# Performance work log

Hardware: AMD Instinct MI355X
Metric: run time of the kernel (lower is better)

## Reference

```python
import jax, jax.numpy as jnp
import numpy as np

N, F_IN, HID, C = 50000, 256, 64, 40
E = 1_600_000
EPS = 1e-8  # torch cosine_similarity eps


def setup_inputs() -> dict:
    key = jax.random.key(0)
    ks = jax.random.split(key, 6)
    x = jax.random.normal(ks[0], (N, F_IN), jnp.float32)
    edge_index = jax.random.randint(ks[1], (2, E), 0, N, dtype=jnp.int64)
    edge_weights = jax.random.uniform(ks[2], (E,), jnp.float32)
    W1 = jax.random.normal(ks[3], (F_IN, HID), jnp.float32) / np.float32(np.sqrt(F_IN))
    b1 = jnp.zeros((HID,), jnp.float32)
    W2 = jax.random.normal(ks[4], (HID, C), jnp.float32) / np.float32(np.sqrt(HID))
    b2 = jnp.zeros((C,), jnp.float32)
    return {"x": x, "edge_index": edge_index, "edge_weights": edge_weights,
            "W1": W1, "b1": b1, "W2": W2, "b2": b2}


def _gcn_conv(x, W, b, src, dst, n):
    # PyG GCNConv: out = D^{-1/2} (A + I) D^{-1/2} (X W) + b
    xw = x @ W  # [n, out]
    loops = jnp.arange(n, dtype=src.dtype)
    s = jnp.concatenate([src, loops])  # self-loops appended
    d = jnp.concatenate([dst, loops])
    deg = jax.ops.segment_sum(jnp.ones_like(s, dtype=xw.dtype), d, num_segments=n)
    dinv = jnp.where(deg > 0, jax.lax.rsqrt(jnp.maximum(deg, 1.0)), 0.0)
    norm = dinv[s] * dinv[d]  # [E+n]
    msg = xw[s] * norm[:, None]  # gather + scale (irregular access)
    out = jax.ops.segment_sum(msg, d, num_segments=n)  # scatter-add
    return out + b


def reference(x, edge_index, edge_weights, W1, b1, W2, b2):
    src, dst = edge_index[0], edge_index[1]
    n = x.shape[0]
    # layer 1 + relu (dropout = identity in eval)
    h = jax.nn.relu(_gcn_conv(x, W1, b1, src, dst, n))
    x_out = _gcn_conv(h, W2, b2, src, dst, n)  # [n, C]
    # edge-wise cosine dissimilarity: 1 - cos(x_out[src], x_out[dst])
    a = x_out[src]
    b = x_out[dst]
    na = jnp.maximum(jnp.sqrt(jnp.sum(a * a, axis=-1)), EPS)
    nb = jnp.maximum(jnp.sqrt(jnp.sum(b * b, axis=-1)), EPS)
    cosine_sim = 1.0 - jnp.sum(a * b, axis=-1) / (na * nb)
    gnn_edge = jnp.where(edge_weights > 0.5, 1.0, -1.0)
    return (jax.nn.log_softmax(x_out, axis=1), x_out, cosine_sim, gnn_edge,
            jax.nn.softmax(x_out, axis=1))
```

## Files before the change

kernel.cpp:

```cpp
#include <hip/hip_runtime.h>
#include <hip/hip_bf16.h>

#define F_IN 256
#define HID  64
#define CLS  40
#define EPS  1e-8f
#define XS_STRIDE 264
#define EPB  8192

typedef unsigned short ushort_t;
typedef unsigned int   uint_t;
typedef __attribute__((ext_vector_type(8))) short bf16x8;
typedef __attribute__((ext_vector_type(4))) float f32x4;

__device__ __forceinline__ float bf2f(ushort_t u) {
    union { uint_t i; float f; } v; v.i = ((uint_t)u) << 16; return v.f;
}
__device__ __forceinline__ ushort_t f2bf(float f) {
    union { float f; uint_t i; } v; v.f = f;
    uint_t r = v.i + 0x7fff + ((v.i >> 16) & 1);
    return (ushort_t)(r >> 16);
}
__device__ __forceinline__ float blo(uint_t p) {
    union { uint_t i; float f; } v; v.i = p << 16; return v.f;
}
__device__ __forceinline__ float bhi(uint_t p) {
    union { uint_t i; float f; } v; v.i = p & 0xffff0000u; return v.f;
}
__device__ __forceinline__ float dot_u4(uint4 a, uint4 b) {
    return blo(a.x) * blo(b.x) + bhi(a.x) * bhi(b.x)
         + blo(a.y) * blo(b.y) + bhi(a.y) * bhi(b.y)
         + blo(a.z) * blo(b.z) + bhi(a.z) * bhi(b.z)
         + blo(a.w) * blo(b.w) + bhi(a.w) * bhi(b.w);
}

__global__ void detect_kernel(const int* __restrict__ raw, int* __restrict__ flag) {
    int c = threadIdx.x;
    int w = raw[2 * c + 1];
    unsigned long long b = __ballot(w != 0);
    if (c == 0) *flag = (b == 0ULL) ? 1 : 0;
}

__global__ void build_hist_kernel(const void* __restrict__ raw, const int* __restrict__ flag,
                                  uint_t* __restrict__ pair, int* __restrict__ ghist, int E) {
    __shared__ int lhist[256];
    int tid = threadIdx.x;
    lhist[tid] = 0;
    __syncthreads();
    int base = blockIdx.x * EPB;
    if (*flag) {
        const long long* r = (const long long*)raw;
        for (int it = 0; it < EPB / 1024; ++it) {
            int e = base + (it * 256 + tid) * 4;
            if (e + 4 <= E) {
                ulonglong2 a0 = *(const ulonglong2*)(r + e);
                ulonglong2 a1 = *(const ulonglong2*)(r + e + 2);
                ulonglong2 b0 = *(const ulonglong2*)(r + E + e);
                ulonglong2 b1 = *(const ulonglong2*)(r + E + e + 2);
                uint_t d0 = (uint_t)b0.x, d1 = (uint_t)b0.y;
                uint_t d2 = (uint_t)b1.x, d3 = (uint_t)b1.y;
                uint4 p;
                p.x = (d0 << 16) | (uint_t)a0.x;
                p.y = (d1 << 16) | (uint_t)a0.y;
                p.z = (d2 << 16) | (uint_t)a1.x;
                p.w = (d3 << 16) | (uint_t)a1.y;
                *(uint4*)(pair + e) = p;
                atomicAdd(&lhist[d0 >> 8], 1);
                atomicAdd(&lhist[d1 >> 8], 1);
                atomicAdd(&lhist[d2 >> 8], 1);
                atomicAdd(&lhist[d3 >> 8], 1);
            } else {
                for (int k = 0; k < 4; ++k) {
                    int ee = e + k;
                    if (ee < E) {
                        uint_t s = (uint_t)r[ee];
                        uint_t d = (uint_t)r[E + ee];
                        pair[ee] = (d << 16) | s;
                        atomicAdd(&lhist[d >> 8], 1);
                    }
                }
            }
        }
    } else {
        const int* r = (const int*)raw;
        for (int it = 0; it < EPB / 1024; ++it) {
            int e = base + (it * 256 + tid) * 4;
            if (e + 4 <= E) {
                int4 a = *(const int4*)(r + e);
                int4 b = *(const int4*)(r + E + e);
                uint_t d0 = (uint_t)b.x, d1 = (uint_t)b.y;
                uint_t d2 = (uint_t)b.z, d3 = (uint_t)b.w;
                uint4 p;
                p.x = (d0 << 16) | (uint_t)a.x;
                p.y = (d1 << 16) | (uint_t)a.y;
                p.z = (d2 << 16) | (uint_t)a.z;
                p.w = (d3 << 16) | (uint_t)a.w;
                *(uint4*)(pair + e) = p;
                atomicAdd(&lhist[d0 >> 8], 1);
                atomicAdd(&lhist[d1 >> 8], 1);
                atomicAdd(&lhist[d2 >> 8], 1);
                atomicAdd(&lhist[d3 >> 8], 1);
            } else {
                for (int k = 0; k < 4; ++k) {
                    int ee = e + k;
                    if (ee < E) {
                        uint_t s = (uint_t)r[ee];
                        uint_t d = (uint_t)r[E + ee];
                        pair[ee] = (d << 16) | s;
                        atomicAdd(&lhist[d >> 8], 1);
                    }
                }
            }
        }
    }
    __syncthreads();
    ghist[blockIdx.x * 256 + tid] = lhist[tid];
}

__global__ void scan_cols_kernel(int* __restrict__ ghist, int* __restrict__ btot,
                                 int NBLK) {
    int k    = blockIdx.x;
    int lane = threadIdx.x;
    int carry = 0;
    for (int b0 = 0; b0 < NBLK; b0 += 64) {
        int b = b0 + lane;
        int v = (b < NBLK) ? ghist[b * 256 + k] : 0;
        int x = v;
        #pragma unroll
        for (int o = 1; o < 64; o <<= 1) {
            int t = __shfl_up(x, o);
            if (lane >= o) x += t;
        }
        if (b < NBLK) ghist[b * 256 + k] = carry + x - v;
        carry += __shfl(x, 63);
    }
    if (lane == 0) btot[k] = carry;
}

__global__ void scan_base_kernel(const int* __restrict__ btot, int* __restrict__ bbase) {
    __shared__ int s[256];
    int k = threadIdx.x;
    int v = btot[k];
    int x = v;
    s[k] = x;
    __syncthreads();
    #pragma unroll
    for (int o = 1; o < 256; o <<= 1) {
        int t = (k >= o) ? s[k - o] : 0;
        __syncthreads();
        x += t;
        s[k] = x;
        __syncthreads();
    }
    bbase[k] = x - v;
    if (k == 255) bbase[256] = x;
}

__global__ void scatter_buckets_kernel(const uint_t* __restrict__ pair,
                                       const int* __restrict__ ghist,
                                       const int* __restrict__ bbase,
                                       uint_t* __restrict__ bkt, int E) {
    __shared__ int cursor[256];
    int tid = threadIdx.x;
    cursor[tid] = ghist[blockIdx.x * 256 + tid] + bbase[tid];
    __syncthreads();
    int base = blockIdx.x * EPB;
    for (int it = 0; it < EPB / 256; ++it) {
        int e = base + it * 256 + tid;
        if (e < E) {
            uint_t u = pair[e];
            int pos = atomicAdd(&cursor[u >> 24], 1);
            bkt[pos] = u;
        }
    }
}

__global__ void bucket_csr_kernel(const uint_t* __restrict__ bkt,
                                  const int* __restrict__ bbase,
                                  ushort_t* __restrict__ csr, int* __restrict__ rowptr,
                                  float* __restrict__ dinv, int n, int E, int NBUCK) {
    __shared__ int lhist[256];
    __shared__ int lscan[256];
    __shared__ int cursor[256];
    int tid = threadIdx.x;
    int kb  = blockIdx.x;
    int base = bbase[kb];
    int cnt  = bbase[kb + 1] - base;
    lhist[tid] = 0;
    __syncthreads();
    for (int i = tid; i < cnt; i += 256) {
        uint_t u = bkt[base + i];
        atomicAdd(&lhist[(u >> 16) & 255], 1);
    }
    __syncthreads();
    int v = lhist[tid];
    int x = v;
    lscan[tid] = x;
    __syncthreads();
    #pragma unroll
    for (int o = 1; o < 256; o <<= 1) {
        int t = (tid >= o) ? lscan[tid - o] : 0;
        __syncthreads();
        x += t;
        lscan[tid] = x;
        __syncthreads();
    }
    int excl = x - v;
    int node = kb * 256 + tid;
    if (node < n) {
        rowptr[node] = base + excl;
        dinv[node]   = rsqrtf((float)(v + 1));
    }
    cursor[tid] = base + excl;
    if (kb == NBUCK - 1 && tid == 0) rowptr[n] = E;
    __syncthreads();
    for (int i = tid; i < cnt; i += 256) {
        uint_t u = bkt[base + i];
        int pos = atomicAdd(&cursor[(u >> 16) & 255], 1);
        csr[pos] = (ushort_t)(u & 0xffffu);
    }
}

__global__ void convert_w1_kernel(const float* __restrict__ W1, ushort_t* __restrict__ W1s) {
    int t = blockIdx.x * blockDim.x + threadIdx.x;
    if (t >= 4 * 8 * 64) return;
    int lane = t & 63;
    int kk   = (t >> 6) & 7;
    int nt   = t >> 9;
    int col  = nt * 16 + (lane & 15);
    int k0   = kk * 32 + (lane >> 4) * 8;
    ushort_t v[8];
    #pragma unroll
    for (int j = 0; j < 8; ++j) v[j] = f2bf(W1[(size_t)(k0 + j) * HID + col]);
    uint4 p;
    p.x = (uint_t)v[0] | ((uint_t)v[1] << 16);
    p.y = (uint_t)v[2] | ((uint_t)v[3] << 16);
    p.z = (uint_t)v[4] | ((uint_t)v[5] << 16);
    p.w = (uint_t)v[6] | ((uint_t)v[7] << 16);
    *(uint4*)(W1s + (size_t)t * 8) = p;
}

__global__ void gemm1_mfma_kernel(const float* __restrict__ x,
                                  const ushort_t* __restrict__ W1s,
                                  const float* __restrict__ dinv,
                                  ushort_t* __restrict__ xws, int n) {
    __shared__ ushort_t xs[16 * XS_STRIDE];
    int node0 = blockIdx.x * 16;
    int tid = threadIdx.x;
    for (int i = tid; i < 16 * 64; i += 256) {
        int r  = i >> 6;
        int c4 = (i & 63) << 2;
        int node = node0 + r;
        float4 v = (node < n) ? *(const float4*)(x + (size_t)node * F_IN + c4)
                              : make_float4(0.f, 0.f, 0.f, 0.f);
        ushort4 b;
        b.x = f2bf(v.x); b.y = f2bf(v.y); b.z = f2bf(v.z); b.w = f2bf(v.w);
        *(ushort4*)(&xs[r * XS_STRIDE + c4]) = b;
    }
    __syncthreads();
    int wave = tid >> 6;
    int lane = tid & 63;
    int m    = lane & 15;
    int q    = lane >> 4;
    f32x4 acc = {0.f, 0.f, 0.f, 0.f};
    #pragma unroll
    for (int kk = 0; kk < 8; ++kk) {
        bf16x8 a = *(const bf16x8*)(&xs[m * XS_STRIDE + kk * 32 + q * 8]);
        bf16x8 b = *(const bf16x8*)(W1s + (((size_t)wave * 8 + kk) * 64 + lane) * 8);
        acc = __builtin_amdgcn_mfma_f32_16x16x32_bf16(a, b, acc, 0, 0, 0);
    }
    int ch = wave * 16 + m;
    #pragma unroll
    for (int r = 0; r < 4; ++r) {
        int node = node0 + q * 4 + r;
        if (node < n)
            xws[(size_t)node * HID + ch] = f2bf(acc[r] * dinv[node]);
    }
}

__global__ void gather1_gemm2_kernel(const int* __restrict__ rowptr,
                                     const ushort_t* __restrict__ csr,
                                     const ushort_t* __restrict__ xws,
                                     const float* __restrict__ dinv,
                                     const float* __restrict__ b1,
                                     const float* __restrict__ W2,
                                     ushort_t* __restrict__ hws, int n) {
    __shared__ float hbuf[4][72];
    __shared__ float w2s[HID * CLS];
    int tid  = threadIdx.x;
    int wave = tid >> 6;
    int l    = tid & 63;
    int g    = l >> 3;
    int lc   = l & 7;
    for (int i = tid; i < HID * CLS / 4; i += 256)
        *(float4*)(&w2s[i * 4]) = *(const float4*)(W2 + i * 4);
    int wv = (blockIdx.x * blockDim.x + tid) >> 6;
    bool active = wv < n;
    int beg = 0, endp = 0;
    float di = 0.f;
    float acc8[8];
    #pragma unroll
    for (int j = 0; j < 8; ++j) acc8[j] = 0.f;
    if (active) {
        beg = rowptr[wv]; endp = rowptr[wv + 1];
        di  = dinv[wv];
        if (l < 8) {
            uint4 sv = *(const uint4*)(xws + (size_t)wv * HID + lc * 8);
            acc8[0] = blo(sv.x); acc8[1] = bhi(sv.x);
            acc8[2] = blo(sv.y); acc8[3] = bhi(sv.y);
            acc8[4] = blo(sv.z); acc8[5] = bhi(sv.z);
            acc8[6] = blo(sv.w); acc8[7] = bhi(sv.w);
        }
    }
    for (int ch = beg; ch < endp; ch += 32) {
        #pragma unroll
        for (int k = 0; k < 4; ++k) {
            int e = ch + k * 8 + g;
            bool val = e < endp;
            int ec = val ? e : (endp - 1);
            int s = (int)csr[ec];
            uint4 p = *(const uint4*)(xws + (size_t)s * HID + lc * 8);
            if (!val) { p.x = 0u; p.y = 0u; p.z = 0u; p.w = 0u; }
            acc8[0] += blo(p.x); acc8[1] += bhi(p.x);
            acc8[2] += blo(p.y); acc8[3] += bhi(p.y);
            acc8[4] += blo(p.z); acc8[5] += bhi(p.z);
            acc8[6] += blo(p.w); acc8[7] += bhi(p.w);
        }
    }
    #pragma unroll
    for (int j = 0; j < 8; ++j) {
        float v = acc8[j];
        v += __shfl_xor(v, 8);
        v += __shfl_xor(v, 16);
        v += __shfl_xor(v, 32);
        acc8[j] = v;
    }
    if (active && l < 8) {
        #pragma unroll
        for (int j = 0; j < 8; ++j)
            hbuf[wave][lc * 8 + j] = fmaxf(acc8[j] * di + b1[lc * 8 + j], 0.f);
    }
    __syncthreads();
    if (active) {
        if (l < CLS) {
            float o = 0.f;
            const float* hr = hbuf[wave];
            #pragma unroll 16
            for (int k = 0; k < HID; ++k) o += hr[k] * w2s[k * CLS + l];
            hws[(size_t)wv * HID + l] = f2bf(o * di);
        } else {
            hws[(size_t)wv * HID + l] = 0;
        }
    }
}

__global__ void gather2_fin_kernel(const int* __restrict__ rowptr,
                                   const ushort_t* __restrict__ csr,
                                   const ushort_t* __restrict__ hws,
                                   const float* __restrict__ dinv,
                                   const float* __restrict__ b2,
                                   float* __restrict__ xout, float* __restrict__ lsm,
                                   float* __restrict__ sm, ushort_t* __restrict__ xnb,
                                   int n) {
    int tid = threadIdx.x;
    int wv  = (blockIdx.x * blockDim.x + tid) >> 6;
    if (wv >= n) return;
    int l  = tid & 63;
    int g  = l >> 3;
    int lc = l & 7;
    int beg = rowptr[wv], endp = rowptr[wv + 1];
    float di = dinv[wv];
    float acc8[8];
    #pragma unroll
    for (int j = 0; j < 8; ++j) acc8[j] = 0.f;
    if (l < 8) {
        uint4 sv = *(const uint4*)(hws + (size_t)wv * HID + lc * 8);
        acc8[0] = blo(sv.x); acc8[1] = bhi(sv.x);
        acc8[2] = blo(sv.y); acc8[3] = bhi(sv.y);
        acc8[4] = blo(sv.z); acc8[5] = bhi(sv.z);
        acc8[6] = blo(sv.w); acc8[7] = bhi(sv.w);
    }
    for (int ch = beg; ch < endp; ch += 32) {
        #pragma unroll
        for (int k = 0; k < 4; ++k) {
            int e = ch + k * 8 + g;
            bool val = e < endp;
            int ec = val ? e : (endp - 1);
            int s = (int)csr[ec];
            uint4 p = *(const uint4*)(hws + (size_t)s * HID + lc * 8);
            if (!val) { p.x = 0u; p.y = 0u; p.z = 0u; p.w = 0u; }
            acc8[0] += blo(p.x); acc8[1] += bhi(p.x);
            acc8[2] += blo(p.y); acc8[3] += bhi(p.y);
            acc8[4] += blo(p.z); acc8[5] += bhi(p.z);
            acc8[6] += blo(p.w); acc8[7] += bhi(p.w);
        }
    }
    #pragma unroll
    for (int j = 0; j < 8; ++j) {
        float v = acc8[j];
        v += __shfl_xor(v, 8);
        v += __shfl_xor(v, 16);
        v += __shfl_xor(v, 32);
        acc8[j] = v;
    }
    bool cgv = lc < 5;
    float raw[8];
    if (cgv) {
        #pragma unroll
        for (int j = 0; j < 8; ++j) raw[j] = acc8[j] * di + b2[lc * 8 + j];
    } else {
        #pragma unroll
        for (int j = 0; j < 8; ++j) raw[j] = 0.f;
    }
    float mx = -3.0e38f;
    if (cgv) {
        #pragma unroll
        for (int j = 0; j < 8; ++j) mx = fmaxf(mx, raw[j]);
    }
    mx = fmaxf(mx, __shfl_xor(mx, 1));
    mx = fmaxf(mx, __shfl_xor(mx, 2));
    mx = fmaxf(mx, __shfl_xor(mx, 4));
    float ex[8];
    float ls = 0.f;
    if (cgv) {
        #pragma unroll
        for (int j = 0; j < 8; ++j) { ex[j] = __expf(raw[j] - mx); ls += ex[j]; }
    } else {
        #pragma unroll
        for (int j = 0; j < 8; ++j) ex[j] = 0.f;
    }
    ls += __shfl_xor(ls, 1);
    ls += __shfl_xor(ls, 2);
    ls += __shfl_xor(ls, 4);
    float sq = 0.f;
    if (cgv) {
        #pragma unroll
        for (int j = 0; j < 8; ++j) sq += raw[j] * raw[j];
    }
    sq += __shfl_xor(sq, 1);
    sq += __shfl_xor(sq, 2);
    sq += __shfl_xor(sq, 4);
    float rn = 1.0f / fmaxf(sqrtf(sq), EPS);
    if (l < 5) {
        size_t fb = (size_t)wv * CLS + l * 8;
        *(float4*)(xout + fb)     = make_float4(raw[0], raw[1], raw[2], raw[3]);
        *(float4*)(xout + fb + 4) = make_float4(raw[4], raw[5], raw[6], raw[7]);
        float lse = mx + __logf(ls);
        *(float4*)(lsm + fb)     = make_float4(raw[0] - lse, raw[1] - lse, raw[2] - lse, raw[3] - lse);
        *(float4*)(lsm + fb + 4) = make_float4(raw[4] - lse, raw[5] - lse, raw[6] - lse, raw[7] - lse);
        float inv = 1.0f / ls;
        *(float4*)(sm + fb)     = make_float4(ex[0] * inv, ex[1] * inv, ex[2] * inv, ex[3] * inv);
        *(float4*)(sm + fb + 4) = make_float4(ex[4] * inv, ex[5] * inv, ex[6] * inv, ex[7] * inv);
        uint4 pb;
        pb.x = (uint_t)f2bf(raw[0] * rn) | ((uint_t)f2bf(raw[1] * rn) << 16);
        pb.y = (uint_t)f2bf(raw[2] * rn) | ((uint_t)f2bf(raw[3] * rn) << 16);
        pb.z = (uint_t)f2bf(raw[4] * rn) | ((uint_t)f2bf(raw[5] * rn) << 16);
        pb.w = (uint_t)f2bf(raw[6] * rn) | ((uint_t)f2bf(raw[7] * rn) << 16);
        *(uint4*)(xnb + fb) = pb;
    }
}

__global__ void edge_kernel(const uint_t* __restrict__ pair,
                            const float* __restrict__ ew, const ushort_t* __restrict__ xnb,
                            float* __restrict__ cos_out, float* __restrict__ gnn_out, int E) {
    int tid = threadIdx.x;
    int wid = (blockIdx.x * blockDim.x + tid) >> 6;
    int l = tid & 63;
    int g = l >> 3;
    int j = l & 7;
    int e0 = wid * 32;
    if (e0 >= E) return;
    uint_t u[4];
    #pragma unroll
    for (int k = 0; k < 4; ++k) {
        int e = e0 + k * 8 + g;
        u[k] = (e < E) ? pair[e] : pair[E - 1];
    }
    uint4 av[4], bv[4];
    #pragma unroll
    for (int k = 0; k < 4; ++k) {
        int s = (int)(u[k] & 0xffffu);
        int d = (int)(u[k] >> 16);
        if (j < 5) {
            av[k] = *(const uint4*)(xnb + (size_t)s * CLS + j * 8);
            bv[k] = *(const uint4*)(xnb + (size_t)d * CLS + j * 8);
        }
    }
    #pragma unroll
    for (int k = 0; k < 4; ++k) {
        float part = 0.f;
        if (j < 5) part = dot_u4(av[k], bv[k]);
        part += __shfl_xor(part, 1);
        part += __shfl_xor(part, 2);
        part += __shfl_xor(part, 4);
        int e = e0 + k * 8 + g;
        if (j == 0 && e < E) {
            cos_out[e] = 1.0f - part;
            gnn_out[e] = (ew[e] > 0.5f) ? 1.0f : -1.0f;
        }
    }
}

extern "C" void kernel_launch(void* const* d_in, const int* in_sizes, int n_in,
                              void* d_out, int out_size, void* d_ws, size_t ws_size,
                              hipStream_t stream) {
    const float* x   = (const float*)d_in[0];
    const void*  ei  = d_in[1];
    const float* ew  = (const float*)d_in[2];
    const float* W1  = (const float*)d_in[3];
    const float* b1  = (const float*)d_in[4];
    const float* W2  = (const float*)d_in[5];
    const float* b2  = (const float*)d_in[6];

    const int n = in_sizes[0] / F_IN;
    const int E = in_sizes[2];

    float* lsm  = (float*)d_out;
    float* xout = lsm + (size_t)n * CLS;
    float* cosO = xout + (size_t)n * CLS;
    float* gnnO = cosO + E;
    float* smO  = gnnO + E;

    char* w = (char*)d_ws;
    auto alloc = [&](size_t bytes) {
        char* p = w;
        w += (bytes + 255) & ~(size_t)255;
        return p;
    };
    const int NBLK  = (E + EPB - 1) / EPB;
    const int NBUCK = (n + 255) / 256;

    uint_t*   pair   = (uint_t*)  alloc((size_t)E * 4);
    uint_t*   bkt    = (uint_t*)  alloc((size_t)E * 4);
    ushort_t* csr16  = (ushort_t*)alloc((size_t)E * 2);
    int*      ghist  = (int*)     alloc((size_t)NBLK * 256 * 4);
    int*      btot   = (int*)     alloc(256 * 4);
    int*      bbase  = (int*)     alloc(257 * 4);
    int*      rowptr = (int*)     alloc(((size_t)n + 1) * 4);
    float*    dinv   = (float*)   alloc((size_t)n * 4);
    ushort_t* xws    = (ushort_t*)alloc((size_t)n * HID * 2);
    ushort_t* hws    = (ushort_t*)alloc((size_t)n * HID * 2);
    ushort_t* xnb    = (ushort_t*)alloc((size_t)n * CLS * 2);
    ushort_t* W1s    = (ushort_t*)alloc((size_t)4 * 8 * 64 * 8 * 2);
    int*      flag   = (int*)     alloc(64);

    detect_kernel<<<1, 64, 0, stream>>>((const int*)ei, flag);
    convert_w1_kernel<<<8, 256, 0, stream>>>(W1, W1s);
    build_hist_kernel<<<NBLK, 256, 0, stream>>>(ei, flag, pair, ghist, E);
    scan_cols_kernel<<<256, 64, 0, stream>>>(ghist, btot, NBLK);
    scan_base_kernel<<<1, 256, 0, stream>>>(btot, bbase);
    scatter_buckets_kernel<<<NBLK, 256, 0, stream>>>(pair, ghist, bbase, bkt, E);
    bucket_csr_kernel<<<NBUCK, 256, 0, stream>>>(bkt, bbase, csr16, rowptr, dinv, n, E, NBUCK);
    gemm1_mfma_kernel<<<(n + 15) / 16, 256, 0, stream>>>(x, W1s, dinv, xws, n);
    gather1_gemm2_kernel<<<((size_t)n * 64 + 255) / 256, 256, 0, stream>>>(rowptr, csr16, xws, dinv,
                                                                           b1, W2, hws, n);
    gather2_fin_kernel<<<((size_t)n * 64 + 255) / 256, 256, 0, stream>>>(rowptr, csr16, hws, dinv, b2,
                                                                         xout, lsm, smO, xnb, n);
    edge_kernel<<<((size_t)((E + 31) / 32) * 64 + 255) / 256, 256, 0, stream>>>(pair, ew, xnb, cosO, gnnO, E);
}
```

Measured before the change: 286.1 us.

## Split gather1 from GEMM2 and run GEMM2 on MFMA bf16

The fused gather1+GEMM2 kernel, which staged W2 (10 KB) into shared memory in every 256-thread block and did a scalar 64x40 dot per node with a block-wide sync, is split in two. A gather-only kernel now writes relu(h) as bf16, and a new MFMA kernel computes h·W2 with W2 pre-packed into bf16 fragments (columns padded to 64). This removes the per-block W2 load and the scalar FMA loop. In exchange it adds one launch plus an extra write and read of an n×64 bf16 intermediate, and h is rounded to bf16 before the second GEMM.

```diff
diff --git a/kernel.cpp b/kernel.cpp
--- a/kernel.cpp
+++ b/kernel.cpp
@@ -6,6 +6,7 @@
 #define CLS  40
 #define EPS  1e-8f
 #define XS_STRIDE 264
+#define H2_STRIDE 72
 #define EPB  8192
 
 typedef unsigned short ushort_t;
@@ -240,6 +241,26 @@
     *(uint4*)(W1s + (size_t)t * 8) = p;
 }
 
+__global__ void convert_w2_kernel(const float* __restrict__ W2, ushort_t* __restrict__ W2s) {
+    int t = blockIdx.x * blockDim.x + threadIdx.x;
+    if (t >= 4 * 2 * 64) return;
+    int lane = t & 63;
+    int kk   = (t >> 6) & 1;
+    int nt   = t >> 7;
+    int col  = nt * 16 + (lane & 15);
+    int k0   = kk * 32 + (lane >> 4) * 8;
+    ushort_t v[8];
+    #pragma unroll
+    for (int j = 0; j < 8; ++j)
+        v[j] = (col < CLS) ? f2bf(W2[(size_t)(k0 + j) * CLS + col]) : (ushort_t)0;
+    uint4 p;
+    p.x = (uint_t)v[0] | ((uint_t)v[1] << 16);
+    p.y = (uint_t)v[2] | ((uint_t)v[3] << 16);
+    p.z = (uint_t)v[4] | ((uint_t)v[5] << 16);
+    p.w = (uint_t)v[6] | ((uint_t)v[7] << 16);
+    *(uint4*)(W2s + (size_t)t * 8) = p;
+}
+
 __global__ void gemm1_mfma_kernel(const float* __restrict__ x,
                                   const ushort_t* __restrict__ W1s,
                                   const float* __restrict__ dinv,
@@ -278,39 +299,29 @@
     }
 }
 
-__global__ void gather1_gemm2_kernel(const int* __restrict__ rowptr,
-                                     const ushort_t* __restrict__ csr,
-                                     const ushort_t* __restrict__ xws,
-                                     const float* __restrict__ dinv,
-                                     const float* __restrict__ b1,
-                                     const float* __restrict__ W2,
-                                     ushort_t* __restrict__ hws, int n) {
-    __shared__ float hbuf[4][72];
-    __shared__ float w2s[HID * CLS];
-    int tid  = threadIdx.x;
-    int wave = tid >> 6;
-    int l    = tid & 63;
-    int g    = l >> 3;
-    int lc   = l & 7;
-    for (int i = tid; i < HID * CLS / 4; i += 256)
-        *(float4*)(&w2s[i * 4]) = *(const float4*)(W2 + i * 4);
-    int wv = (blockIdx.x * blockDim.x + tid) >> 6;
-    bool active = wv < n;
-    int beg = 0, endp = 0;
-    float di = 0.f;
+__global__ void gather1_kernel(const int* __restrict__ rowptr,
+                               const ushort_t* __restrict__ csr,
+                               const ushort_t* __restrict__ xws,
+                               const float* __restrict__ dinv,
+                               const float* __restrict__ b1,
+                               ushort_t* __restrict__ h, int n) {
+    int tid = threadIdx.x;
+    int wv  = (blockIdx.x * blockDim.x + tid) >> 6;
+    if (wv >= n) return;
+    int l  = tid & 63;
+    int g  = l >> 3;
+    int lc = l & 7;
+    int beg = rowptr[wv], endp = rowptr[wv + 1];
+    float di = dinv[wv];
     float acc8[8];
     #pragma unroll
     for (int j = 0; j < 8; ++j) acc8[j] = 0.f;
-    if (active) {
-        beg = rowptr[wv]; endp = rowptr[wv + 1];
-        di  = dinv[wv];
-        if (l < 8) {
-            uint4 sv = *(const uint4*)(xws + (size_t)wv * HID + lc * 8);
-            acc8[0] = blo(sv.x); acc8[1] = bhi(sv.x);
-            acc8[2] = blo(sv.y); acc8[3] = bhi(sv.y);
-            acc8[4] = blo(sv.z); acc8[5] = bhi(sv.z);
-            acc8[6] = blo(sv.w); acc8[7] = bhi(sv.w);
-        }
+    if (l < 8) {
+        uint4 sv = *(const uint4*)(xws + (size_t)wv * HID + lc * 8);
+        acc8[0] = blo(sv.x); acc8[1] = bhi(sv.x);
+        acc8[2] = blo(sv.y); acc8[3] = bhi(sv.y);
+        acc8[4] = blo(sv.z); acc8[5] = bhi(sv.z);
+        acc8[6] = blo(sv.w); acc8[7] = bhi(sv.w);
     }
     for (int ch = beg; ch < endp; ch += 32) {
         #pragma unroll
@@ -335,22 +346,59 @@
         v += __shfl_xor(v, 32);
         acc8[j] = v;
     }
-    if (active && l < 8) {
-        #pragma unroll
-        for (int j = 0; j < 8; ++j)
-            hbuf[wave][lc * 8 + j] = fmaxf(acc8[j] * di + b1[lc * 8 + j], 0.f);
-    }
-    __syncthreads();
-    if (active) {
-        if (l < CLS) {
-            float o = 0.f;
-            const float* hr = hbuf[wave];
-            #pragma unroll 16
-            for (int k = 0; k < HID; ++k) o += hr[k] * w2s[k * CLS + l];
-            hws[(size_t)wv * HID + l] = f2bf(o * di);
-        } else {
-            hws[(size_t)wv * HID + l] = 0;
-        }
+    if (l < 8) {
+        float4 bb0 = *(const float4*)(b1 + lc * 8);
+        float4 bb1 = *(const float4*)(b1 + lc * 8 + 4);
+        float h0 = fmaxf(acc8[0] * di + bb0.x, 0.f);
+        float h1 = fmaxf(acc8[1] * di + bb0.y, 0.f);
+        float h2 = fmaxf(acc8[2] * di + bb0.z, 0.f);
+        float h3 = fmaxf(acc8[3] * di + bb0.w, 0.f);
+        float h4 = fmaxf(acc8[4] * di + bb1.x, 0.f);
+        float h5 = fmaxf(acc8[5] * di + bb1.y, 0.f);
+        float h6 = fmaxf(acc8[6] * di + bb1.z, 0.f);
+        float h7 = fmaxf(acc8[7] * di + bb1.w, 0.f);
+        uint4 pb;
+        pb.x = (uint_t)f2bf(h0) | ((uint_t)f2bf(h1) << 16);
+        pb.y = (uint_t)f2bf(h2) | ((uint_t)f2bf(h3) << 16);
+        pb.z = (uint_t)f2bf(h4) | ((uint_t)f2bf(h5) << 16);
+        pb.w = (uint_t)f2bf(h6) | ((uint_t)f2bf(h7) << 16);
+        *(uint4*)(h + (size_t)wv * HID + lc * 8) = pb;
+    }
+}
+
+__global__ void gemm2_mfma_kernel(const ushort_t* __restrict__ h,
+                                  const ushort_t* __restrict__ W2s,
+                                  const float* __restrict__ dinv,
+                                  ushort_t* __restrict__ hws, int n) {
+    __shared__ ushort_t hs[16 * H2_STRIDE];
+    int node0 = blockIdx.x * 16;
+    int tid = threadIdx.x;
+    {
+        int r  = tid >> 4;
+        int c4 = (tid & 15) << 2;
+        int node = node0 + r;
+        ushort4 v = make_ushort4(0, 0, 0, 0);
+        if (node < n) v = *(const ushort4*)(h + (size_t)node * HID + c4);
+        *(ushort4*)(&hs[r * H2_STRIDE + c4]) = v;
+    }
+    __syncthreads();
+    int wave = tid >> 6;
+    int lane = tid & 63;
+    int m    = lane & 15;
+    int q    = lane >> 4;
+    f32x4 acc = {0.f, 0.f, 0.f, 0.f};
+    #pragma unroll
+    for (int kk = 0; kk < 2; ++kk) {
+        bf16x8 a = *(const bf16x8*)(&hs[m * H2_STRIDE + kk * 32 + q * 8]);
+        bf16x8 b = *(const bf16x8*)(W2s + (((size_t)wave * 2 + kk) * 64 + lane) * 8);
+        acc = __builtin_amdgcn_mfma_f32_16x16x32_bf16(a, b, acc, 0, 0, 0);
+    }
+    int ch = wave * 16 + m;
+    #pragma unroll
+    for (int r = 0; r < 4; ++r) {
+        int node = node0 + q * 4 + r;
+        if (node < n)
+            hws[(size_t)node * HID + ch] = f2bf(acc[r] * dinv[node]);
     }
 }
 
@@ -539,21 +587,25 @@
     int*      rowptr = (int*)     alloc(((size_t)n + 1) * 4);
     float*    dinv   = (float*)   alloc((size_t)n * 4);
     ushort_t* xws    = (ushort_t*)alloc((size_t)n * HID * 2);
+    ushort_t* hbuf   = (ushort_t*)alloc((size_t)n * HID * 2);
     ushort_t* hws    = (ushort_t*)alloc((size_t)n * HID * 2);
     ushort_t* xnb    = (ushort_t*)alloc((size_t)n * CLS * 2);
     ushort_t* W1s    = (ushort_t*)alloc((size_t)4 * 8 * 64 * 8 * 2);
+    ushort_t* W2s    = (ushort_t*)alloc((size_t)4 * 2 * 64 * 8 * 2);
     int*      flag   = (int*)     alloc(64);
 
     detect_kernel<<<1, 64, 0, stream>>>((const int*)ei, flag);
     convert_w1_kernel<<<8, 256, 0, stream>>>(W1, W1s);
+    convert_w2_kernel<<<2, 256, 0, stream>>>(W2, W2s);
     build_hist_kernel<<<NBLK, 256, 0, stream>>>(ei, flag, pair, ghist, E);
     scan_cols_kernel<<<256, 64, 0, stream>>>(ghist, btot, NBLK);
     scan_base_kernel<<<1, 256, 0, stream>>>(btot, bbase);
     scatter_buckets_kernel<<<NBLK, 256, 0, stream>>>(pair, ghist, bbase, bkt, E);
     bucket_csr_kernel<<<NBUCK, 256, 0, stream>>>(bkt, bbase, csr16, rowptr, dinv, n, E, NBUCK);
     gemm1_mfma_kernel<<<(n + 15) / 16, 256, 0, stream>>>(x, W1s, dinv, xws, n);
-    gather1_gemm2_kernel<<<((size_t)n * 64 + 255) / 256, 256, 0, stream>>>(rowptr, csr16, xws, dinv,
-                                                                           b1, W2, hws, n);
+    gather1_kernel<<<((size_t)n * 64 + 255) / 256, 256, 0, stream>>>(rowptr, csr16, xws, dinv,
+                                                                     b1, hbuf, n);
+    gemm2_mfma_kernel<<<(n + 15) / 16, 256, 0, stream>>>(hbuf, W2s, dinv, hws, n);
     gather2_fin_kernel<<<((size_t)n * 64 + 255) / 256, 256, 0, stream>>>(rowptr, csr16, hws, dinv, b2,
                                                                          xout, lsm, smO, xnb, n);
     edge_kernel<<<((size_t)((E + 31) / 32) * 64 + 255) / 256, 256, 0, stream>>>(pair, ew, xnb, cosO, gnnO, E);
```

Result: no change. 281.8 us (-1.5%).
